# Optimization experiments

Measured on AMD Instinct MI355X. Metric: run time of the kernel, lower is better.

## Reference

```python
import jax, jax.numpy as jnp
import numpy as np

N = 100000   # nodes
D = 128      # in_ft == out_ft (residual mix requires equality)
E = 1600000  # edges (nnz of sparse A)


def setup_inputs() -> dict:
    key = jax.random.key(0)
    ks = jax.random.split(key, 8)
    X = jax.random.normal(ks[0], (N, D), dtype=jnp.float32)   # unused by forward math, kept for fidelity
    X0 = jax.random.normal(ks[1], (N, D), dtype=jnp.float32)
    row = jnp.sort(jax.random.randint(ks[2], (E,), 0, N))      # sparse A row indices (sorted)
    col = jax.random.randint(ks[3], (E,), 0, N)                # sparse A col indices
    vals = jax.random.uniform(ks[4], (E,), dtype=jnp.float32)  # sparse A values
    # nn.Linear(D, D): weight [out, in], bias [out]
    bound = 1.0 / np.sqrt(D)
    W = jax.random.uniform(ks[5], (D, D), minval=-bound, maxval=bound, dtype=jnp.float32)
    b = jax.random.uniform(ks[6], (D,), minval=-bound, maxval=bound, dtype=jnp.float32)
    alpha = jax.random.uniform(ks[7], (), dtype=jnp.float32)
    beta = jax.random.uniform(jax.random.fold_in(key, 7), (), dtype=jnp.float32)
    return {"X": X, "X0": X0, "row": row, "col": col, "vals": vals,
            "W": W, "b": b, "alpha": alpha, "beta": beta}


def reference(X, X0, row, col, vals, W, b, alpha, beta):
    # SpMM: (A @ X0)[i] = sum_e vals[e] * X0[col[e]] for edges with row[e] == i
    AX0 = jax.ops.segment_sum(vals[:, None] * X0[col], row, num_segments=N)  # [N, D]
    Xi = (1.0 - alpha) * AX0 + alpha * X0
    out = (1.0 - beta) * Xi + beta * (Xi @ W.T + b)
    return out
```

## Files before the change

kernel.cpp:

```cpp
#include <hip/hip_runtime.h>

#define D_FT 128

__device__ inline unsigned f2bf(float f) {
    unsigned u = __float_as_uint(f);
    return (u + 0x7FFFu + ((u >> 16) & 1u)) >> 16;
}
__device__ inline unsigned pack2bf(float a, float b) {
    return f2bf(a) | (f2bf(b) << 16);
}

typedef __attribute__((ext_vector_type(4))) float f32x4;
typedef __attribute__((ext_vector_type(8))) short bf16x8;

__global__ __launch_bounds__(256) void build_row_ptr_kernel(
    const int* __restrict__ row, int* __restrict__ ptr, int n_edges, int n_nodes)
{
    const int e = blockIdx.x * 256 + threadIdx.x;
    if (e > n_edges) return;
    const int lo = (e == 0) ? 0 : row[e - 1] + 1;
    const int hi = (e == n_edges) ? n_nodes : row[e];
    for (int i = lo; i <= hi; ++i) ptr[i] = e;
}

template<bool USE_PTR>
__global__ __launch_bounds__(256) void spmm_mix_kernel(
    const float* __restrict__ X0,
    const int*   __restrict__ row,
    const int*   __restrict__ col,
    const float* __restrict__ vals,
    const int*   __restrict__ row_ptr,
    const float* __restrict__ alpha_p,
    float*       __restrict__ Xi,
    int n_nodes, int n_edges)
{
    const int wave = threadIdx.x >> 6;
    const int lane = threadIdx.x & 63;
    const int node = blockIdx.x * 4 + wave;
    if (node >= n_nodes) return;

    int ebeg, eend;
    if (USE_PTR) {
        ebeg = row_ptr[node];
        eend = row_ptr[node + 1];
    } else {
        int lo0 = 0, hi0 = n_edges, lo1 = 0, hi1 = n_edges;
        while ((lo0 < hi0) || (lo1 < hi1)) {
            int m0 = (lo0 + hi0) >> 1; if (m0 >= n_edges) m0 = n_edges - 1;
            int m1 = (lo1 + hi1) >> 1; if (m1 >= n_edges) m1 = n_edges - 1;
            const int r0v = row[m0];
            const int r1v = row[m1];
            if (lo0 < hi0) { if (r0v < node)     lo0 = m0 + 1; else hi0 = m0; }
            if (lo1 < hi1) { if (r1v < node + 1) lo1 = m1 + 1; else hi1 = m1; }
        }
        ebeg = lo0; eend = lo1;
    }

    const int d0 = lane * 2;
    float ax = 0.f, ay = 0.f;

    for (int e = ebeg; e < eend; e += 64) {
        const int n = min(64, eend - e);
        int   cl = 0; float vl = 0.f;
        if (lane < n) { cl = col[e + lane]; vl = vals[e + lane]; }
        for (int j0 = 0; j0 < n; j0 += 8) {
            float2 xs[8]; float vv[8];
            #pragma unroll
            for (int j = 0; j < 8; ++j) {
                const int c = __shfl(cl, j0 + j);
                vv[j] = __shfl(vl, j0 + j);
                xs[j] = *(const float2*)(X0 + (size_t)c * D_FT + d0);
            }
            #pragma unroll
            for (int j = 0; j < 8; ++j) {
                ax += vv[j] * xs[j].x;
                ay += vv[j] * xs[j].y;
            }
        }
    }

    const float alpha = *alpha_p;
    const float2 x0self = *(const float2*)(X0 + (size_t)node * D_FT + d0);
    float2 xi;
    xi.x = (1.f - alpha) * ax + alpha * x0self.x;
    xi.y = (1.f - alpha) * ay + alpha * x0self.y;
    *(float2*)(Xi + (size_t)node * D_FT + d0) = xi;
}

__global__ __launch_bounds__(256) void gemm_mix_kernel(
    const float* __restrict__ W,
    const float* __restrict__ bias,
    const float* __restrict__ beta_p,
    float*       __restrict__ io,
    int n_nodes)
{
    __shared__ __align__(16) char lds_raw[65536];
    char* __restrict__ ldsA = lds_raw;
    char* __restrict__ ldsB = lds_raw + 32768;

    const int t  = threadIdx.x;
    const int r0 = blockIdx.x * 128;

    #pragma unroll
    for (int i = 0; i < 16; ++i) {
        const int f4 = i * 256 + t;
        const int r  = f4 >> 5;
        const int c4 = f4 & 31;
        int gr = r0 + r; if (gr >= n_nodes) gr = n_nodes - 1;
        const float4 x = *(const float4*)(io + (size_t)gr * D_FT + c4 * 4);
        uint2 v; v.x = pack2bf(x.x, x.y); v.y = pack2bf(x.z, x.w);
        int byte = r * 256 + c4 * 8;
        byte ^= (r & 7) << 4;
        *(uint2*)(ldsA + byte) = v;
    }
    #pragma unroll
    for (int i = 0; i < 16; ++i) {
        const int f4 = i * 256 + t;
        const int o  = f4 >> 5;
        const int c4 = f4 & 31;
        const float4 x = *(const float4*)(W + (size_t)o * D_FT + c4 * 4);
        uint2 v; v.x = pack2bf(x.x, x.y); v.y = pack2bf(x.z, x.w);
        int byte = o * 256 + c4 * 8;
        byte ^= (o & 7) << 4;
        *(uint2*)(ldsB + byte) = v;
    }
    __syncthreads();

    const int w   = t >> 6;
    const int l   = t & 63;
    const int lhi = l >> 4;
    const int llo = l & 15;

    f32x4 acc[2][8];
    #pragma unroll
    for (int m = 0; m < 2; ++m)
        #pragma unroll
        for (int n = 0; n < 8; ++n)
            acc[m][n] = (f32x4){0.f, 0.f, 0.f, 0.f};

    #pragma unroll
    for (int ks = 0; ks < 4; ++ks) {
        const int kb = ks * 64 + lhi * 16;
        bf16x8 a[2], b[8];
        #pragma unroll
        for (int m = 0; m < 2; ++m) {
            const int r = w * 32 + m * 16 + llo;
            int byte = r * 256 + kb;
            byte ^= (r & 7) << 4;
            a[m] = *(const bf16x8*)(ldsA + byte);
        }
        #pragma unroll
        for (int n = 0; n < 8; ++n) {
            const int o = n * 16 + llo;
            int byte = o * 256 + kb;
            byte ^= (o & 7) << 4;
            b[n] = *(const bf16x8*)(ldsB + byte);
        }
        #pragma unroll
        for (int m = 0; m < 2; ++m)
            #pragma unroll
            for (int n = 0; n < 8; ++n)
                acc[m][n] = __builtin_amdgcn_mfma_f32_16x16x32_bf16(
                    a[m], b[n], acc[m][n], 0, 0, 0);
    }

    const float beta = *beta_p;
    const float ob = 1.f - beta;
    float bb[8];
    #pragma unroll
    for (int n = 0; n < 8; ++n) bb[n] = bias[n * 16 + llo];

    #pragma unroll
    for (int m = 0; m < 2; ++m) {
        const int rbase = r0 + w * 32 + m * 16 + lhi * 4;
        #pragma unroll
        for (int q = 0; q < 4; ++q) {
            const int R = rbase + q;
            if (R < n_nodes) {
                #pragma unroll
                for (int n = 0; n < 8; ++n) {
                    const int C = n * 16 + llo;
                    const float xi = io[(size_t)R * D_FT + C];
                    io[(size_t)R * D_FT + C] = ob * xi + beta * (acc[m][n][q] + bb[n]);
                }
            }
        }
    }
}

extern "C" void kernel_launch(void* const* d_in, const int* in_sizes, int n_in,
                              void* d_out, int out_size, void* d_ws, size_t ws_size,
                              hipStream_t stream) {
    const float* X0    = (const float*)d_in[1];
    const int*   row   = (const int*)  d_in[2];
    const int*   col   = (const int*)  d_in[3];
    const float* vals  = (const float*)d_in[4];
    const float* W     = (const float*)d_in[5];
    const float* b     = (const float*)d_in[6];
    const float* alpha = (const float*)d_in[7];
    const float* beta  = (const float*)d_in[8];
    float* out = (float*)d_out;

    const int n_nodes = in_sizes[1] / D_FT;
    const int n_edges = in_sizes[2];

    const size_t ptr_bytes = (size_t)(n_nodes + 1) * sizeof(int);
    const bool use_ptr = (ws_size >= ptr_bytes);

    if (use_ptr) {
        int* row_ptr = (int*)d_ws;
        build_row_ptr_kernel<<<(n_edges + 256) / 256, 256, 0, stream>>>(
            row, row_ptr, n_edges, n_nodes);
        spmm_mix_kernel<true><<<(n_nodes + 3) / 4, 256, 0, stream>>>(
            X0, row, col, vals, row_ptr, alpha, out, n_nodes, n_edges);
    } else {
        spmm_mix_kernel<false><<<(n_nodes + 3) / 4, 256, 0, stream>>>(
            X0, row, col, vals, nullptr, alpha, out, n_nodes, n_edges);
    }
    gemm_mix_kernel<<<(n_nodes + 127) / 128, 256, 0, stream>>>(
        W, b, beta, out, n_nodes);
}
```

Measured before the change: 274.9 us.

## Load GEMM A operand directly to registers and stage outputs via LDS

The GEMM kernel now loads each wave's A fragment straight from global memory into registers and converts it to bf16 in place, so the A tile no longer goes through LDS. LDS drops to 32KB and tiles shrink to 64 rows, which allows more blocks per CU. The accumulators are staged back through LDS so the epilogue does coalesced float4 read-modify-writes instead of scalar strided ones. The SpMM gather loop is also unrolled to 16 edges per batch to keep more loads in flight, at the cost of more registers and wasted work on rows with few edges.

```diff
diff --git a/kernel.cpp b/kernel.cpp
--- a/kernel.cpp
+++ b/kernel.cpp
@@ -12,6 +12,8 @@
 
 typedef __attribute__((ext_vector_type(4))) float f32x4;
 typedef __attribute__((ext_vector_type(8))) short bf16x8;
+
+union bf8u { bf16x8 v; unsigned u[4]; };
 
 __global__ __launch_bounds__(256) void build_row_ptr_kernel(
     const int* __restrict__ row, int* __restrict__ ptr, int n_edges, int n_nodes)
@@ -63,16 +65,16 @@
         const int n = min(64, eend - e);
         int   cl = 0; float vl = 0.f;
         if (lane < n) { cl = col[e + lane]; vl = vals[e + lane]; }
-        for (int j0 = 0; j0 < n; j0 += 8) {
-            float2 xs[8]; float vv[8];
+        for (int j0 = 0; j0 < n; j0 += 16) {
+            float2 xs[16]; float vv[16];
             #pragma unroll
-            for (int j = 0; j < 8; ++j) {
+            for (int j = 0; j < 16; ++j) {
                 const int c = __shfl(cl, j0 + j);
                 vv[j] = __shfl(vl, j0 + j);
                 xs[j] = *(const float2*)(X0 + (size_t)c * D_FT + d0);
             }
             #pragma unroll
-            for (int j = 0; j < 8; ++j) {
+            for (int j = 0; j < 16; ++j) {
                 ax += vv[j] * xs[j].x;
                 ay += vv[j] * xs[j].y;
             }
@@ -94,25 +96,28 @@
     float*       __restrict__ io,
     int n_nodes)
 {
-    __shared__ __align__(16) char lds_raw[65536];
-    char* __restrict__ ldsA = lds_raw;
-    char* __restrict__ ldsB = lds_raw + 32768;
-
-    const int t  = threadIdx.x;
-    const int r0 = blockIdx.x * 128;
-
-    #pragma unroll
-    for (int i = 0; i < 16; ++i) {
-        const int f4 = i * 256 + t;
-        const int r  = f4 >> 5;
-        const int c4 = f4 & 31;
-        int gr = r0 + r; if (gr >= n_nodes) gr = n_nodes - 1;
-        const float4 x = *(const float4*)(io + (size_t)gr * D_FT + c4 * 4);
-        uint2 v; v.x = pack2bf(x.x, x.y); v.y = pack2bf(x.z, x.w);
-        int byte = r * 256 + c4 * 8;
-        byte ^= (r & 7) << 4;
-        *(uint2*)(ldsA + byte) = v;
-    }
+    __shared__ __align__(16) char lds_raw[32768];
+    char*  __restrict__ ldsB = lds_raw;
+    float* __restrict__ ldsS = (float*)lds_raw;
+
+    const int t   = threadIdx.x;
+    const int w   = t >> 6;
+    const int l   = t & 63;
+    const int lhi = l >> 4;
+    const int llo = l & 15;
+    const int r0  = blockIdx.x * 64;
+
+    int arow = r0 + w * 16 + llo;
+    if (arow >= n_nodes) arow = n_nodes - 1;
+    const float* aptr = io + (size_t)arow * D_FT;
+    float4 af0[4], af1[4];
+    #pragma unroll
+    for (int ks = 0; ks < 4; ++ks) {
+        const int k0 = ks * 32 + lhi * 8;
+        af0[ks] = *(const float4*)(aptr + k0);
+        af1[ks] = *(const float4*)(aptr + k0 + 4);
+    }
+
     #pragma unroll
     for (int i = 0; i < 16; ++i) {
         const int f4 = i * 256 + t;
@@ -126,64 +131,58 @@
     }
     __syncthreads();
 
-    const int w   = t >> 6;
-    const int l   = t & 63;
-    const int lhi = l >> 4;
-    const int llo = l & 15;
-
-    f32x4 acc[2][8];
-    #pragma unroll
-    for (int m = 0; m < 2; ++m)
-        #pragma unroll
-        for (int n = 0; n < 8; ++n)
-            acc[m][n] = (f32x4){0.f, 0.f, 0.f, 0.f};
+    f32x4 acc[8];
+    #pragma unroll
+    for (int n = 0; n < 8; ++n) acc[n] = (f32x4){0.f, 0.f, 0.f, 0.f};
 
     #pragma unroll
     for (int ks = 0; ks < 4; ++ks) {
+        bf8u a;
+        a.u[0] = pack2bf(af0[ks].x, af0[ks].y);
+        a.u[1] = pack2bf(af0[ks].z, af0[ks].w);
+        a.u[2] = pack2bf(af1[ks].x, af1[ks].y);
+        a.u[3] = pack2bf(af1[ks].z, af1[ks].w);
         const int kb = ks * 64 + lhi * 16;
-        bf16x8 a[2], b[8];
-        #pragma unroll
-        for (int m = 0; m < 2; ++m) {
-            const int r = w * 32 + m * 16 + llo;
-            int byte = r * 256 + kb;
-            byte ^= (r & 7) << 4;
-            a[m] = *(const bf16x8*)(ldsA + byte);
-        }
         #pragma unroll
         for (int n = 0; n < 8; ++n) {
             const int o = n * 16 + llo;
             int byte = o * 256 + kb;
             byte ^= (o & 7) << 4;
-            b[n] = *(const bf16x8*)(ldsB + byte);
-        }
+            const bf16x8 b = *(const bf16x8*)(ldsB + byte);
+            acc[n] = __builtin_amdgcn_mfma_f32_16x16x32_bf16(a.v, b, acc[n], 0, 0, 0);
+        }
+    }
+
+    __syncthreads();
+    #pragma unroll
+    for (int n = 0; n < 8; ++n) {
+        const int C = n * 16 + llo;
+        const int rt = w * 16 + lhi * 4;
         #pragma unroll
-        for (int m = 0; m < 2; ++m)
-            #pragma unroll
-            for (int n = 0; n < 8; ++n)
-                acc[m][n] = __builtin_amdgcn_mfma_f32_16x16x32_bf16(
-                    a[m], b[n], acc[m][n], 0, 0, 0);
-    }
+        for (int q = 0; q < 4; ++q)
+            ldsS[(rt + q) * 128 + C] = acc[n][q];
+    }
+    __syncthreads();
 
     const float beta = *beta_p;
     const float ob = 1.f - beta;
-    float bb[8];
-    #pragma unroll
-    for (int n = 0; n < 8; ++n) bb[n] = bias[n * 16 + llo];
-
-    #pragma unroll
-    for (int m = 0; m < 2; ++m) {
-        const int rbase = r0 + w * 32 + m * 16 + lhi * 4;
-        #pragma unroll
-        for (int q = 0; q < 4; ++q) {
-            const int R = rbase + q;
-            if (R < n_nodes) {
-                #pragma unroll
-                for (int n = 0; n < 8; ++n) {
-                    const int C = n * 16 + llo;
-                    const float xi = io[(size_t)R * D_FT + C];
-                    io[(size_t)R * D_FT + C] = ob * xi + beta * (acc[m][n][q] + bb[n]);
-                }
-            }
+    const int c4 = t & 31;
+    const int rb = t >> 5;
+    const float4 bb = *(const float4*)(bias + c4 * 4);
+
+    #pragma unroll
+    for (int i = 0; i < 8; ++i) {
+        const int r  = rb * 8 + i;
+        const int gr = r0 + r;
+        if (gr < n_nodes) {
+            const float4 a4  = *(const float4*)(ldsS + r * 128 + c4 * 4);
+            const float4 xi4 = *(const float4*)(io + (size_t)gr * D_FT + c4 * 4);
+            float4 o;
+            o.x = ob * xi4.x + beta * (a4.x + bb.x);
+            o.y = ob * xi4.y + beta * (a4.y + bb.y);
+            o.z = ob * xi4.z + beta * (a4.z + bb.z);
+            o.w = ob * xi4.w + beta * (a4.w + bb.w);
+            *(float4*)(io + (size_t)gr * D_FT + c4 * 4) = o;
         }
     }
 }
@@ -217,6 +216,6 @@
         spmm_mix_kernel<false><<<(n_nodes + 3) / 4, 256, 0, stream>>>(
             X0, row, col, vals, nullptr, alpha, out, n_nodes, n_edges);
     }
-    gemm_mix_kernel<<<(n_nodes + 127) / 128, 256, 0, stream>>>(
+    gemm_mix_kernel<<<(n_nodes + 63) / 64, 256, 0, stream>>>(
         W, b, beta, out, n_nodes);
 }
```

After: 274.9 us. About the same (-0.0%).
